# Kernel optimization log

Measured on AMD Instinct MI355X. Metric: run time of the kernel, lower is better.

## Reference

```python
import jax, jax.numpy as jnp
import numpy as np

SIGMA = 1.0
E_THETA = 0.1
E_ALPHA = 1.0
T = 750   # hardcoded loop length in the original module
W = 11    # window width
B = 4096


def _pad(x):
    # matches: pad[:, :6]=x[:,0]; pad[:, 6:-5]=x; pad[:, -6:]=x[:,-1]
    # (index T+5 is written twice with the same value -> net layout: 6 left, 5 right)
    return jnp.concatenate(
        [jnp.repeat(x[:, :1], 6, axis=1), x, jnp.repeat(x[:, -1:], 5, axis=1)], axis=1
    )


def setup_inputs() -> dict:
    key = jax.random.key(0)
    k1, k2 = jax.random.split(key)
    actioness = jax.random.uniform(k1, (B, T), dtype=jnp.float32)
    actioness_2 = jax.random.uniform(k2, (B, T), dtype=jnp.float32)
    return {"actioness": actioness, "actioness_2": actioness_2}


def reference(actioness, actioness_2):
    a3 = _pad(actioness_2)   # [B, T+11]
    a4 = _pad(actioness)     # [B, T+11]
    idx = jnp.arange(T)[:, None] + jnp.arange(W)[None, :]  # [T, W], window i..i+10
    a4w = jax.lax.stop_gradient(a4[:, idx])  # [B, T, W] (detached in original)
    a3w = jax.lax.stop_gradient(a3[:, idx])  # [B, T, W]

    d = actioness[:, :, None] - a4w          # [B, T, W]
    # torch.norm(..., dim=0)**2 == sum over batch dim -> scalar weight per (i, j)
    w = jnp.exp(-jnp.sum(d * d, axis=0) / (2.0 * SIGMA * SIGMA))  # [T, W]

    # sum over (i, j) of batch-mean of w_ij * |a2[:,i] - a3[:,i+j]|
    loss = jnp.sum(jnp.mean(w[None, :, :] * jnp.abs(actioness_2[:, :, None] - a3w), axis=0))

    res = actioness - actioness_2
    loss = loss + jnp.mean(E_THETA * jnp.sum(res * res, axis=1))
    return loss * E_ALPHA
```

## Files before the change

kernel.cpp:

```cpp
#include <hip/hip_runtime.h>

#define BATCH  4096
#define TLEN   750
#define NK     6
#define WSTRIP 250
#define NSTRIP 3
#define NTH1   768
#define RSUB   4
#define NGR    256
#define RPB    (BATCH/NGR)
#define RPW    (RPB/RSUB)
#define QSZ    (2*NK*256)
#define NJ     (NSTRIP*NK*2)
#define NTH2   1024


template<int NW>
__device__ __forceinline__ float block_reduce(float v, float* red) {
    #pragma unroll
    for (int off = 32; off > 0; off >>= 1) v += __shfl_down(v, off, 64);
    const int t = threadIdx.x;
    if ((t & 63) == 0) red[t >> 6] = v;
    __syncthreads();
    float r = 0.f;
    if (t == 0) {
        #pragma unroll
        for (int w = 0; w < NW; ++w) r += red[w];
    }
    __syncthreads();
    return r;
}

__global__ __launch_bounds__(NTH1, 3) void actloss_k1(
        const float* __restrict__ a, const float* __restrict__ a2,
        float* __restrict__ p, float* __restrict__ resp) {
    const int t  = threadIdx.x;
    const int w  = t >> 6;
    const int l  = t & 63;
    const int s  = w % NSTRIP;
    const int rw = w / NSTRIP;
    const int g  = (int)blockIdx.x;

    const int colr = s * WSTRIP + 4 * l;
    const int bc0  = min(colr,     TLEN - 2);
    const int bc1  = min(colr + 2, TLEN - 2);

    float maskf[4];
    #pragma unroll
    for (int c = 0; c < 4; ++c) maskf[c] = (4 * l + c < WSTRIP) ? 1.f : 0.f;

    float s1[4][NK], s2[4][NK];
    #pragma unroll
    for (int c = 0; c < 4; ++c)
        #pragma unroll
        for (int k = 0; k < NK; ++k) { s1[c][k] = 0.f; s2[c][k] = 0.f; }
    float res = 0.f;

    const int r0 = g * RPB + rw * RPW;
    #pragma unroll
    for (int r = 0; r < RPW; ++r) {
        const size_t off = (size_t)(r0 + r) * TLEN;
        const float2 av0 = *reinterpret_cast<const float2*>(a  + off + bc0);
        const float2 av1 = *reinterpret_cast<const float2*>(a  + off + bc1);
        const float2 bv0 = *reinterpret_cast<const float2*>(a2 + off + bc0);
        const float2 bv1 = *reinterpret_cast<const float2*>(a2 + off + bc1);

        float n[10], m[10];
        n[0] = av0.x; n[1] = av0.y; n[2] = av1.x; n[3] = av1.y;
        m[0] = bv0.x; m[1] = bv0.y; m[2] = bv1.x; m[3] = bv1.y;
        #pragma unroll
        for (int j = 0; j < 4; ++j) {
            n[4 + j] = __shfl_down(n[j], 1, 64);
            m[4 + j] = __shfl_down(m[j], 1, 64);
        }
        n[8] = __shfl_down(n[0], 2, 64);  n[9] = __shfl_down(n[1], 2, 64);
        m[8] = __shfl_down(m[0], 2, 64);  m[9] = __shfl_down(m[1], 2, 64);

        #pragma unroll
        for (int c = 0; c < 4; ++c) {
            #pragma unroll
            for (int k = 1; k <= NK; ++k) {
                const float d = n[c] - n[c + k];
                s1[c][k - 1] = fmaf(d, d, s1[c][k - 1]);
                s2[c][k - 1] += fabsf(m[c] - m[c + k]);
            }
            const float rr = n[c] - m[c];
            res = fmaf(rr * rr, maskf[c], res);
        }
    }

    __shared__ float buf[NSTRIP][QSZ];
    __shared__ float rwred[12];
    if (rw == 0) {
        #pragma unroll
        for (int k = 0; k < NK; ++k) {
            *reinterpret_cast<float4*>(&buf[s][k * 256 + 4 * l]) =
                make_float4(s1[0][k], s1[1][k], s1[2][k], s1[3][k]);
            *reinterpret_cast<float4*>(&buf[s][NK * 256 + k * 256 + 4 * l]) =
                make_float4(s2[0][k], s2[1][k], s2[2][k], s2[3][k]);
        }
    }
    #pragma unroll
    for (int off = 32; off > 0; off >>= 1) res += __shfl_down(res, off, 64);
    if (l == 0) rwred[w] = res;
    __syncthreads();
    #pragma unroll
    for (int stage = 1; stage < RSUB; ++stage) {
        if (rw == stage) {
            #pragma unroll
            for (int k = 0; k < NK; ++k) {
                float4* q1 = reinterpret_cast<float4*>(&buf[s][k * 256 + 4 * l]);
                float4 v1 = *q1;
                v1.x += s1[0][k]; v1.y += s1[1][k]; v1.z += s1[2][k]; v1.w += s1[3][k];
                *q1 = v1;
                float4* q2 = reinterpret_cast<float4*>(&buf[s][NK * 256 + k * 256 + 4 * l]);
                float4 v2 = *q2;
                v2.x += s2[0][k]; v2.y += s2[1][k]; v2.z += s2[2][k]; v2.w += s2[3][k];
                *q2 = v2;
            }
        }
        __syncthreads();
    }

    for (int q = t; q < NSTRIP * QSZ; q += NTH1) {
        const int si  = q / QSZ;
        const int qq  = q % QSZ;
        const float v = buf[si][qq];
        const int arr = qq >= (NK * 256);
        const int rem = qq - arr * (NK * 256);
        const int k   = rem >> 8;
        const int col = rem & 255;
        const int h   = col >> 7;
        const int idx = (col & 127) + arr * 128;
        const int j   = si * 12 + (k << 1) + h;
        p[((size_t)j * NGR + g) * 256 + idx] = v;
    }
    if (t == 0) {
        float rs = 0.f;
        #pragma unroll
        for (int i = 0; i < 12; ++i) rs += rwred[i];
        resp[g] = rs;
    }
}

__global__ __launch_bounds__(NTH2) void actloss_k2(
        const float* __restrict__ p, float* __restrict__ partial) {
    const int t = threadIdx.x;
    const int j = (int)blockIdx.x;
    const float4* slab = reinterpret_cast<const float4*>(p + (size_t)j * NGR * 256);

    float4 acc4 = make_float4(0.f, 0.f, 0.f, 0.f);
    #pragma unroll
    for (int pass = 0; pass < NGR / 16; ++pass) {
        const float4 v = slab[pass * 1024 + t];
        acc4.x += v.x; acc4.y += v.y; acc4.z += v.z; acc4.w += v.w;
    }

    __shared__ float buf[16][256];
    __shared__ float sm[256];
    __shared__ float red[16];
    const int w  = t >> 6;
    const int sl = 4 * (t & 63);
    *reinterpret_cast<float4*>(&buf[w][sl]) = acc4;
    __syncthreads();
    if (t < 256) {
        float v = 0.f;
        #pragma unroll
        for (int w2 = 0; w2 < 16; ++w2) v += buf[w2][t];
        sm[t] = v;
    }
    __syncthreads();

    float acc = 0.f;
    if (t < 128) {
        const int s  = j / 12;
        const int jj = j % 12;
        const int k1 = (jj >> 1) + 1;
        const int h  = jj & 1;
        const int col = h * 128 + t;
        const int i   = s * WSTRIP + col;
        if (col < WSTRIP && i + k1 <= TLEN - 1) {
            const float Tv = expf(-0.5f * sm[t]) * sm[t + 128];
            float wgt = (k1 <= 4) ? 2.f : 1.f;
            if (i == 0) wgt += (float)(6 - k1);
            if (k1 <= 3 && i == TLEN - 1 - k1) wgt += (float)(4 - k1);
            acc = wgt * Tv;
        }
    }
    const float r = block_reduce<16>(acc, red);
    if (t == 0) partial[j] = r;
}

__global__ __launch_bounds__(256) void actloss_k3(
        const float* __restrict__ partial, const float* __restrict__ resp,
        float* __restrict__ out) {
    const int t = threadIdx.x;
    __shared__ float red[4];
    const float pa = (t < NJ) ? partial[t] : 0.f;
    const float ra = resp[t];
    const float paR = block_reduce<4>(pa, red);
    const float raR = block_reduce<4>(ra, red);
    if (t == 0) out[0] = (paR + 0.1f * raR) * (1.0f / (float)BATCH);
}


__global__ __launch_bounds__(256) void actloss_col_kernel(
        const float* __restrict__ a, const float* __restrict__ a2,
        float* __restrict__ part) {
    const int i = blockIdx.x;
    const int t = threadIdx.x;
    __shared__ float red[4];
    int cidx[11];
    #pragma unroll
    for (int j = 0; j < 11; ++j) {
        int c = i + j - 6;
        cidx[j] = c < 0 ? 0 : (c > TLEN - 1 ? TLEN - 1 : c);
    }
    float s1[11], s2[11];
    #pragma unroll
    for (int j = 0; j < 11; ++j) { s1[j] = 0.f; s2[j] = 0.f; }
    float resacc = 0.f;
    for (int b = t; b < BATCH; b += 256) {
        const float* arow  = a  + (size_t)b * TLEN;
        const float* a2row = a2 + (size_t)b * TLEN;
        const float ai = arow[i], a2i = a2row[i];
        const float r = ai - a2i;
        resacc = fmaf(r, r, resacc);
        #pragma unroll
        for (int j = 0; j < 11; ++j) {
            const float d = ai - arow[cidx[j]];
            s1[j] = fmaf(d, d, s1[j]);
            s2[j] += fabsf(a2i - a2row[cidx[j]]);
        }
    }
    float term = 0.f;
    #pragma unroll
    for (int j = 0; j < 11; ++j) {
        const float s1r = block_reduce<4>(s1[j], red);
        const float s2r = block_reduce<4>(s2[j], red);
        if (t == 0) term += expf(-0.5f * s1r) * s2r;
    }
    const float resr = block_reduce<4>(resacc, red);
    if (t == 0) part[i] = (term + 0.1f * resr) * (1.0f / (float)BATCH);
}

__global__ __launch_bounds__(256) void actloss_fallback_reduce(
        const float* __restrict__ part, float* __restrict__ out) {
    __shared__ float red[4];
    float v = 0.f;
    for (int k = threadIdx.x; k < TLEN; k += 256) v += part[k];
    const float r = block_reduce<4>(v, red);
    if (threadIdx.x == 0) out[0] = r;
}


extern "C" void kernel_launch(void* const* d_in, const int* in_sizes, int n_in,
                              void* d_out, int out_size, void* d_ws, size_t ws_size,
                              hipStream_t stream) {
    const float* a  = (const float*)d_in[0];
    const float* a2 = (const float*)d_in[1];
    float* out = (float*)d_out;
    float* ws  = (float*)d_ws;

    const size_t pN   = (size_t)NJ * NGR * 256;
    const size_t need = (pN + 64 + NGR + 16) * sizeof(float);

    if (ws_size >= need) {
        float* p       = ws;
        float* partial = p + pN;
        float* resp    = partial + 64;
        actloss_k1<<<NGR,  NTH1, 0, stream>>>(a, a2, p, resp);
        actloss_k2<<<NJ,   NTH2, 0, stream>>>(p, partial);
        actloss_k3<<<1,    256,  0, stream>>>(partial, resp, out);
    } else {
        float* part = ws;
        actloss_col_kernel<<<TLEN, 256, 0, stream>>>(a, a2, part);
        actloss_fallback_reduce<<<1, 256, 0, stream>>>(part, out);
    }
}
```

Before: 22.88 us.

## Pack per-block partial sums as bf16 pairs and hoist row loads in k1

The first kernel now rounds each pair of per-block column partial sums (squared-difference and absolute-difference) to bf16 and packs them into one 32-bit word. This halves the workspace traffic between the first and second kernels, and the second kernel's reduction layout is reorganised to match. All row loads in k1 are issued before any compute so the memory latency overlaps, and the resp reduction moves into k2 so k3 becomes a single wavefront. Truncating the partial sums to bf16 lowers the accuracy of the loss, and holding all loaded rows at once raises register pressure.

After: 19.55 us. -14.6%, faster.

```diff
diff --git a/kernel.cpp b/kernel.cpp
--- a/kernel.cpp
+++ b/kernel.cpp
@@ -31,9 +31,15 @@
     return r;
 }
 
+__device__ __forceinline__ unsigned pack2(float v1, float v2) {
+    const unsigned b1 = (__float_as_uint(v1) + 0x8000u) >> 16;
+    const unsigned b2 = (__float_as_uint(v2) + 0x8000u) >> 16;
+    return (b1 << 16) | (b2 & 0xffffu);
+}
+
 __global__ __launch_bounds__(NTH1, 3) void actloss_k1(
         const float* __restrict__ a, const float* __restrict__ a2,
-        float* __restrict__ p, float* __restrict__ resp) {
+        unsigned* __restrict__ pu, float* __restrict__ resp) {
     const int t  = threadIdx.x;
     const int w  = t >> 6;
     const int l  = t & 63;
@@ -57,17 +63,22 @@
     float res = 0.f;
 
     const int r0 = g * RPB + rw * RPW;
+
+    float2 A0[RPW], A1[RPW], B0[RPW], B1[RPW];
     #pragma unroll
     for (int r = 0; r < RPW; ++r) {
         const size_t off = (size_t)(r0 + r) * TLEN;
-        const float2 av0 = *reinterpret_cast<const float2*>(a  + off + bc0);
-        const float2 av1 = *reinterpret_cast<const float2*>(a  + off + bc1);
-        const float2 bv0 = *reinterpret_cast<const float2*>(a2 + off + bc0);
-        const float2 bv1 = *reinterpret_cast<const float2*>(a2 + off + bc1);
-
+        A0[r] = *reinterpret_cast<const float2*>(a  + off + bc0);
+        A1[r] = *reinterpret_cast<const float2*>(a  + off + bc1);
+        B0[r] = *reinterpret_cast<const float2*>(a2 + off + bc0);
+        B1[r] = *reinterpret_cast<const float2*>(a2 + off + bc1);
+    }
+
+    #pragma unroll
+    for (int r = 0; r < RPW; ++r) {
         float n[10], m[10];
-        n[0] = av0.x; n[1] = av0.y; n[2] = av1.x; n[3] = av1.y;
-        m[0] = bv0.x; m[1] = bv0.y; m[2] = bv1.x; m[3] = bv1.y;
+        n[0] = A0[r].x; n[1] = A0[r].y; n[2] = A1[r].x; n[3] = A1[r].y;
+        m[0] = B0[r].x; m[1] = B0[r].y; m[2] = B1[r].x; m[3] = B1[r].y;
         #pragma unroll
         for (int j = 0; j < 4; ++j) {
             n[4 + j] = __shfl_down(n[j], 1, 64);
@@ -122,18 +133,16 @@
         __syncthreads();
     }
 
-    for (int q = t; q < NSTRIP * QSZ; q += NTH1) {
-        const int si  = q / QSZ;
-        const int qq  = q % QSZ;
-        const float v = buf[si][qq];
-        const int arr = qq >= (NK * 256);
-        const int rem = qq - arr * (NK * 256);
+    for (int e = t; e < NSTRIP * NK * 256; e += NTH1) {
+        const int si  = e / (NK * 256);
+        const int rem = e % (NK * 256);
         const int k   = rem >> 8;
         const int col = rem & 255;
         const int h   = col >> 7;
-        const int idx = (col & 127) + arr * 128;
-        const int j   = si * 12 + (k << 1) + h;
-        p[((size_t)j * NGR + g) * 256 + idx] = v;
+        const int idx = col & 127;
+        const unsigned pk = pack2(buf[si][k * 256 + col],
+                                  buf[si][NK * 256 + k * 256 + col]);
+        pu[((size_t)(si * 12 + (k << 1) + h) * NGR + g) * 128 + idx] = pk;
     }
     if (t == 0) {
         float rs = 0.f;
@@ -144,35 +153,42 @@
 }
 
 __global__ __launch_bounds__(NTH2) void actloss_k2(
-        const float* __restrict__ p, float* __restrict__ partial) {
+        const unsigned* __restrict__ pu, const float* __restrict__ resp,
+        float* __restrict__ partial) {
     const int t = threadIdx.x;
     const int j = (int)blockIdx.x;
-    const float4* slab = reinterpret_cast<const float4*>(p + (size_t)j * NGR * 256);
-
-    float4 acc4 = make_float4(0.f, 0.f, 0.f, 0.f);
-    #pragma unroll
-    for (int pass = 0; pass < NGR / 16; ++pass) {
-        const float4 v = slab[pass * 1024 + t];
-        acc4.x += v.x; acc4.y += v.y; acc4.z += v.z; acc4.w += v.w;
-    }
-
-    __shared__ float buf[16][256];
-    __shared__ float sm[256];
+    const uint4* slab = reinterpret_cast<const uint4*>(pu + (size_t)j * NGR * 128);
+
+    const int cg    = t & 31;
+    const int gbase = t >> 5;
+
+    float s1a[4] = {0.f, 0.f, 0.f, 0.f}, s2a[4] = {0.f, 0.f, 0.f, 0.f};
+    #pragma unroll
+    for (int pass = 0; pass < NGR / 32; ++pass) {
+        const uint4 v = slab[(size_t)(pass * 32 + gbase) * 32 + cg];
+        const unsigned u[4] = {v.x, v.y, v.z, v.w};
+        #pragma unroll
+        for (int c = 0; c < 4; ++c) {
+            s1a[c] += __uint_as_float(u[c] & 0xffff0000u);
+            s2a[c] += __uint_as_float(u[c] << 16);
+        }
+    }
+
+    __shared__ float smA[NTH2][5], smB[NTH2][5];
     __shared__ float red[16];
-    const int w  = t >> 6;
-    const int sl = 4 * (t & 63);
-    *reinterpret_cast<float4*>(&buf[w][sl]) = acc4;
-    __syncthreads();
-    if (t < 256) {
-        float v = 0.f;
-        #pragma unroll
-        for (int w2 = 0; w2 < 16; ++w2) v += buf[w2][t];
-        sm[t] = v;
-    }
+    #pragma unroll
+    for (int c = 0; c < 4; ++c) { smA[t][c] = s1a[c]; smB[t][c] = s2a[c]; }
     __syncthreads();
 
     float acc = 0.f;
     if (t < 128) {
+        float S1 = 0.f, S2 = 0.f;
+        const int rcg = t >> 2, ci = t & 3;
+        #pragma unroll
+        for (int q = 0; q < 32; ++q) {
+            S1 += smA[q * 32 + rcg][ci];
+            S2 += smB[q * 32 + rcg][ci];
+        }
         const int s  = j / 12;
         const int jj = j % 12;
         const int k1 = (jj >> 1) + 1;
@@ -180,7 +196,7 @@
         const int col = h * 128 + t;
         const int i   = s * WSTRIP + col;
         if (col < WSTRIP && i + k1 <= TLEN - 1) {
-            const float Tv = expf(-0.5f * sm[t]) * sm[t + 128];
+            const float Tv = expf(-0.5f * S1) * S2;
             float wgt = (k1 <= 4) ? 2.f : 1.f;
             if (i == 0) wgt += (float)(6 - k1);
             if (k1 <= 3 && i == TLEN - 1 - k1) wgt += (float)(4 - k1);
@@ -189,18 +205,22 @@
     }
     const float r = block_reduce<16>(acc, red);
     if (t == 0) partial[j] = r;
-}
-
-__global__ __launch_bounds__(256) void actloss_k3(
-        const float* __restrict__ partial, const float* __restrict__ resp,
-        float* __restrict__ out) {
-    const int t = threadIdx.x;
-    __shared__ float red[4];
-    const float pa = (t < NJ) ? partial[t] : 0.f;
-    const float ra = resp[t];
-    const float paR = block_reduce<4>(pa, red);
-    const float raR = block_reduce<4>(ra, red);
-    if (t == 0) out[0] = (paR + 0.1f * raR) * (1.0f / (float)BATCH);
+
+    if (j == 0) {
+        const float ra = (t < NGR) ? resp[t] : 0.f;
+        const float r2 = block_reduce<16>(ra, red);
+        if (t == 0) partial[NJ] = r2;
+    }
+}
+
+__global__ __launch_bounds__(64) void actloss_k3(
+        const float* __restrict__ partial, float* __restrict__ out) {
+    const int t = threadIdx.x;
+    float v = (t < NJ) ? partial[t] : 0.f;
+    if (t == 0) v += 0.1f * partial[NJ];
+    #pragma unroll
+    for (int off = 32; off > 0; off >>= 1) v += __shfl_down(v, off, 64);
+    if (t == 0) out[0] = v * (1.0f / (float)BATCH);
 }
 
 
@@ -260,20 +280,19 @@
     const float* a  = (const float*)d_in[0];
     const float* a2 = (const float*)d_in[1];
     float* out = (float*)d_out;
-    float* ws  = (float*)d_ws;
-
-    const size_t pN   = (size_t)NJ * NGR * 256;
-    const size_t need = (pN + 64 + NGR + 16) * sizeof(float);
+
+    const size_t puN  = (size_t)NJ * NGR * 128;
+    const size_t need = (puN + 64 + NGR + 16) * 4;
 
     if (ws_size >= need) {
-        float* p       = ws;
-        float* partial = p + pN;
-        float* resp    = partial + 64;
-        actloss_k1<<<NGR,  NTH1, 0, stream>>>(a, a2, p, resp);
-        actloss_k2<<<NJ,   NTH2, 0, stream>>>(p, partial);
-        actloss_k3<<<1,    256,  0, stream>>>(partial, resp, out);
+        unsigned* pu      = (unsigned*)d_ws;
+        float*    partial = (float*)(pu + puN);
+        float*    resp    = partial + 64;
+        actloss_k1<<<NGR, NTH1, 0, stream>>>(a, a2, pu, resp);
+        actloss_k2<<<NJ,  NTH2, 0, stream>>>(pu, resp, partial);
+        actloss_k3<<<1,   64,   0, stream>>>(partial, out);
     } else {
-        float* part = ws;
+        float* part = (float*)d_ws;
         actloss_col_kernel<<<TLEN, 256, 0, stream>>>(a, a2, part);
         actloss_fallback_reduce<<<1, 256, 0, stream>>>(part, out);
     }
```
